# Kernel optimization log

Measured on AMD Instinct MI355X. Metric: run time of the kernel, lower is better.

The kernel has to match this reference:

```python
import jax, jax.numpy as jnp
import numpy as np

B, S, D = 4, 4096, 256

def setup_inputs() -> dict:
    key = jax.random.key(0)
    ks = jax.random.split(key, 7)
    s = 1.0 / np.sqrt(D)
    return {
        "x": jax.random.normal(ks[0], (B, S, D), dtype=jnp.float32),
        "Wq": jax.random.normal(ks[1], (D, D), dtype=jnp.float32) * s,
        "bq": jax.random.normal(ks[2], (D,), dtype=jnp.float32) * s,
        "Wk": jax.random.normal(ks[3], (D, D), dtype=jnp.float32) * s,
        "bk": jax.random.normal(ks[4], (D,), dtype=jnp.float32) * s,
        "Wv": jax.random.normal(ks[5], (D, D), dtype=jnp.float32) * s,
        "bv": jax.random.normal(ks[6], (D,), dtype=jnp.float32) * s,
    }

def reference(x, Wq, bq, Wk, bk, Wv, bv):
    # nn.Linear: y = x @ W.T + b
    q = jnp.einsum('bsd,ed->bse', x, Wq) + bq  # [B,S,D]
    k = jnp.einsum('bsd,ed->bse', x, Wk) + bk  # [B,S,D]
    v = jnp.einsum('bsd,ed->bse', x, Wv) + bv  # [B,S,D]
    scale = 1.0 / jnp.sqrt(jnp.float32(x.shape[-1]))
    scores = jnp.einsum('bqd,bkd->bqk', q, k) * scale  # [B,S,S]
    attn = jax.nn.softmax(scores, axis=-1)
    return jnp.einsum('bqk,bkd->bqd', attn, v)
```

## Files before the change

kernel.cpp:

```cpp
#include <hip/hip_runtime.h>

typedef __attribute__((ext_vector_type(8))) short bf16x8;
typedef __attribute__((ext_vector_type(4))) short bf16x4;
typedef __attribute__((ext_vector_type(4))) float f32x4;
typedef __attribute__((ext_vector_type(16))) float f32x16;

#define MFMA16(a,b,c) __builtin_amdgcn_mfma_f32_16x16x32_bf16((a),(b),(c),0,0,0)
#define MFMA32(a,b,c) __builtin_amdgcn_mfma_f32_32x32x16_bf16((a),(b),(c),0,0,0)

__device__ __forceinline__ short f2bf(float f) {
  union { float f; unsigned u; } v; v.f = f;
  unsigned r = v.u + 0x7FFFu + ((v.u >> 16) & 1u);
  return (short)(r >> 16);
}

__device__ __forceinline__ void async16(const void* g, void* l) {
  __builtin_amdgcn_global_load_lds(
      (const __attribute__((address_space(1))) unsigned*)g,
      (__attribute__((address_space(3))) unsigned*)l, 16, 0, 0);
}

__global__ void cvt_w_kernel(const float* __restrict__ Wq, const float* __restrict__ Wk,
                             const float* __restrict__ Wv, short* __restrict__ Wb) {
  int v = blockIdx.x * 256 + threadIdx.x;
  int z = v >> 13, r = v & 8191;
  const float* src = ((z == 0) ? Wq : (z == 1) ? Wk : Wv) + r * 8;
  float4 a = *(const float4*)src;
  float4 b = *(const float4*)(src + 4);
  bf16x8 h;
  h[0]=f2bf(a.x); h[1]=f2bf(a.y); h[2]=f2bf(a.z); h[3]=f2bf(a.w);
  h[4]=f2bf(b.x); h[5]=f2bf(b.y); h[6]=f2bf(b.z); h[7]=f2bf(b.w);
  *(bf16x8*)(Wb + z * 65536 + r * 8) = h;
}

__global__ __launch_bounds__(256, 1) void proj_kernel(
    const float* __restrict__ x, const short* __restrict__ Wb,
    const float* __restrict__ bq, const float* __restrict__ bk, const float* __restrict__ bv,
    short* __restrict__ Qb, short* __restrict__ Kb, short* __restrict__ VTb)
{
  __shared__ __attribute__((aligned(16))) char xs[32768];
  const int tid = threadIdx.x;
  const int lane = tid & 63;
  const int w = tid >> 6;
  const int l15 = lane & 15, lg = lane >> 4;
  const int m0 = blockIdx.x * 64;
  const int batch = m0 >> 12;
  const int s0 = m0 & 4095;

  #pragma unroll
  for (int c = 0; c < 8; ++c) {
    int v = c * 256 + tid;
    int row = v >> 5, u = v & 31;
    const float* g = x + (size_t)(m0 + row) * 256 + u * 8;
    float4 a = *(const float4*)g;
    float4 b = *(const float4*)(g + 4);
    bf16x8 h;
    h[0]=f2bf(a.x); h[1]=f2bf(a.y); h[2]=f2bf(a.z); h[3]=f2bf(a.w);
    h[4]=f2bf(b.x); h[5]=f2bf(b.y); h[6]=f2bf(b.z); h[7]=f2bf(b.w);
    *(bf16x8*)(xs + row * 512 + ((u ^ (row & 7)) * 16)) = h;
  }
  __syncthreads();

  for (int z = 0; z < 2; ++z) {
    const short* Wz = Wb + z * 65536;
    const float* bias = z ? bk : bq;
    short* Ob = z ? Kb : Qb;
    const float scl = z ? 1.0f : 0.0625f;
    bf16x8 wf[4][8];
    #pragma unroll
    for (int fc = 0; fc < 4; ++fc)
      #pragma unroll
      for (int ks = 0; ks < 8; ++ks)
        wf[fc][ks] = *(const bf16x8*)(Wz + (size_t)(w*64 + fc*16 + l15) * 256 + ks*32 + lg*8);
    float bb[4];
    #pragma unroll
    for (int fc = 0; fc < 4; ++fc) bb[fc] = bias[w*64 + fc*16 + l15];
    #pragma unroll
    for (int ms = 0; ms < 4; ++ms) {
      bf16x8 xa[8];
      #pragma unroll
      for (int ks = 0; ks < 8; ++ks) {
        int row = ms * 16 + l15;
        xa[ks] = *(const bf16x8*)(xs + row * 512 + (((ks*4 + lg) ^ (row & 7)) * 16));
      }
      f32x4 acc[4];
      #pragma unroll
      for (int fc = 0; fc < 4; ++fc) acc[fc] = (f32x4){0.f,0.f,0.f,0.f};
      #pragma unroll
      for (int ks = 0; ks < 8; ++ks)
        #pragma unroll
        for (int fc = 0; fc < 4; ++fc)
          acc[fc] = MFMA16(xa[ks], wf[fc][ks], acc[fc]);
      #pragma unroll
      for (int fc = 0; fc < 4; ++fc)
        #pragma unroll
        for (int r = 0; r < 4; ++r)
          Ob[(size_t)(m0 + ms*16 + lg*4 + r) * 256 + w*64 + fc*16 + l15] =
              f2bf((acc[fc][r] + bb[fc]) * scl);
    }
  }

  {
    const short* Wz = Wb + 2 * 65536;
    bf16x8 wf[4][8];
    #pragma unroll
    for (int fr = 0; fr < 4; ++fr)
      #pragma unroll
      for (int ks = 0; ks < 8; ++ks)
        wf[fr][ks] = *(const bf16x8*)(Wz + (size_t)(w*64 + fr*16 + l15) * 256 + ks*32 + lg*8);
    float bvr[4][4];
    #pragma unroll
    for (int fr = 0; fr < 4; ++fr)
      #pragma unroll
      for (int r = 0; r < 4; ++r) bvr[fr][r] = bv[w*64 + fr*16 + lg*4 + r];
    #pragma unroll
    for (int ms = 0; ms < 4; ++ms) {
      bf16x8 xa[8];
      #pragma unroll
      for (int ks = 0; ks < 8; ++ks) {
        int row = ms * 16 + l15;
        xa[ks] = *(const bf16x8*)(xs + row * 512 + (((ks*4 + lg) ^ (row & 7)) * 16));
      }
      f32x4 acc[4];
      #pragma unroll
      for (int fr = 0; fr < 4; ++fr) acc[fr] = (f32x4){0.f,0.f,0.f,0.f};
      #pragma unroll
      for (int ks = 0; ks < 8; ++ks)
        #pragma unroll
        for (int fr = 0; fr < 4; ++fr)
          acc[fr] = MFMA16(wf[fr][ks], xa[ks], acc[fr]);
      #pragma unroll
      for (int fr = 0; fr < 4; ++fr)
        #pragma unroll
        for (int r = 0; r < 4; ++r) {
          int e = w*64 + fr*16 + lg*4 + r;
          VTb[(size_t)(batch*256 + e) * 4096 + s0 + ms*16 + l15] = f2bf(acc[fr][r] + bvr[fr][r]);
        }
    }
  }
}

__global__ __launch_bounds__(512, 2) void attn_kernel(
    const short* __restrict__ Qb, const short* __restrict__ Kb,
    const short* __restrict__ VTb, float* __restrict__ Op, float* __restrict__ mlg)
{
  __shared__ __attribute__((aligned(16))) char smem[148480];
  const int tid = threadIdx.x;
  const int lane = tid & 63;
  const int w = tid >> 6;
  const int l31 = lane & 31, hi = lane >> 5;
  const int qs = w & 3, kh = w >> 2, dh = kh;

  const int b = blockIdx.x;
  const int xcd = b & 7;
  const int batch = xcd >> 1, ns = xcd & 1;
  const int qt = b >> 3;
  const int q0 = qt * 128;
  const int kvbase = ns * 2048;

  const char* Kg = (const char*)(Kb  + (size_t)batch * 4096 * 256);
  const char* Vg = (const char*)(VTb + (size_t)batch * 256 * 4096);

  bf16x8 qf[16];
  {
    const short* qrow = Qb + (size_t)(batch*4096 + q0 + qs*32 + l31) * 256;
    #pragma unroll
    for (int ks = 0; ks < 16; ++ks) qf[ks] = *(const bf16x8*)(qrow + ks*16 + hi*8);
  }

  f32x16 o[4];
  #pragma unroll
  for (int i = 0; i < 4; ++i)
    #pragma unroll
    for (int r = 0; r < 16; ++r) o[i][r] = 0.f;
  float m_run = -1e30f, l_run = 0.f;

  float* ml = (float*)(smem + 147456);
  char* pl = smem + 131072 + qs * 4096;

  auto stage = [&](int buf, int kv0) {
    char* kl = smem + buf * 32768;
    #pragma unroll
    for (int c = 0; c < 4; ++c) {
      int v = c * 512 + tid;
      int row = v >> 5, s = v & 31;
      async16(Kg + (size_t)(kv0 + row) * 512 + ((s ^ (row & 7)) * 16),
              kl + (c * 512 + w * 64) * 16);
    }
    char* vl = smem + 65536 + buf * 32768;
    #pragma unroll
    for (int c = 0; c < 4; ++c) {
      int v = c * 512 + tid;
      int row = v >> 3, s = v & 7;
      async16(Vg + (size_t)row * 8192 + (size_t)kv0 * 2 + ((s ^ (row & 7)) * 16),
              vl + (c * 512 + w * 64) * 16);
    }
  };

  stage(0, kvbase);
  __syncthreads();

  for (int t = 0; t < 32; ++t) {
    const int cur = t & 1;
    if (t < 31) stage(cur ^ 1, kvbase + (t + 1) * 64);

    const char* kl = smem + cur * 32768;
    const char* vl = smem + 65536 + cur * 32768;

    f32x16 st;
    #pragma unroll
    for (int r = 0; r < 16; ++r) st[r] = 0.f;
    #pragma unroll
    for (int ks = 0; ks < 16; ++ks) {
      int row = kh * 32 + l31;
      bf16x8 kf = *(const bf16x8*)(kl + row * 512 + (((ks*2 + hi) ^ (row & 7)) * 16));
      st = MFMA32(kf, qf[ks], st);
    }

    float mx = st[0];
    #pragma unroll
    for (int r = 1; r < 16; ++r) mx = fmaxf(mx, st[r]);
    mx = fmaxf(mx, __shfl_xor(mx, 32));
    if (!hi) ml[kh * 128 + qs * 32 + l31] = mx;
    asm volatile("s_waitcnt lgkmcnt(0)" ::: "memory");
    __builtin_amdgcn_s_barrier();
    float mo = ml[(kh ^ 1) * 128 + qs * 32 + l31];
    float m_new = fmaxf(m_run, fmaxf(mx, mo));
    if (m_new > m_run) {
      float alpha = __expf(m_run - m_new);
      l_run *= alpha;
      #pragma unroll
      for (int df = 0; df < 4; ++df) o[df] = o[df] * alpha;
      m_run = m_new;
    }
    float ps[16];
    float lsum = 0.f;
    #pragma unroll
    for (int r = 0; r < 16; ++r) { ps[r] = __expf(st[r] - m_run); lsum += ps[r]; }
    l_run += lsum;
    #pragma unroll
    for (int g = 0; g < 4; ++g) {
      bf16x4 pv;
      #pragma unroll
      for (int j = 0; j < 4; ++j) pv[j] = f2bf(ps[4*g + j]);
      int qd = kh * 8 + 2 * g + hi;
      int u8 = qd ^ ((l31 & 7) << 1);
      *(bf16x4*)(pl + l31 * 128 + u8 * 8) = pv;
    }
    asm volatile("s_waitcnt lgkmcnt(0)" ::: "memory");
    __builtin_amdgcn_s_barrier();

    #pragma unroll
    for (int ks = 0; ks < 4; ++ks) {
      int u8 = (ks * 4 + hi * 2) ^ ((l31 & 7) << 1);
      bf16x8 pa = *(const bf16x8*)(pl + l31 * 128 + u8 * 8);
      #pragma unroll
      for (int df = 0; df < 4; ++df) {
        int row = dh * 128 + df * 32 + l31;
        bf16x8 vb = *(const bf16x8*)(vl + row * 128 + (((ks*2 + hi) ^ (row & 7)) * 16));
        o[df] = MFMA32(vb, pa, o[df]);
      }
    }
    __syncthreads();
  }

  float lw = l_run + __shfl_xor(l_run, 32);
  if (!hi) ml[kh * 128 + qs * 32 + l31] = lw;
  asm volatile("s_waitcnt lgkmcnt(0)" ::: "memory");
  __builtin_amdgcn_s_barrier();
  float lt = ml[qs * 32 + l31] + ml[128 + qs * 32 + l31];
  const int qglob = batch * 4096 + q0 + qs * 32 + l31;
  float* op = Op + ((size_t)ns * 16384 + qglob) * 256;
  #pragma unroll
  for (int df = 0; df < 4; ++df)
    #pragma unroll
    for (int g = 0; g < 4; ++g) {
      float4 vv = {o[df][4*g], o[df][4*g+1], o[df][4*g+2], o[df][4*g+3]};
      *(float4*)(op + dh * 128 + df * 32 + 8 * g + 4 * hi) = vv;
    }
  if (kh == 0 && !hi) {
    mlg[((size_t)ns * 16384 + qglob) * 2]     = m_run;
    mlg[((size_t)ns * 16384 + qglob) * 2 + 1] = lt;
  }
}

__global__ void combine_kernel(const float* __restrict__ Op, const float* __restrict__ mlg,
                               float* __restrict__ out) {
  int idx = blockIdx.x * 256 + threadIdx.x;
  int row = idx >> 6, c = idx & 63;
  float m0 = mlg[row * 2],           l0 = mlg[row * 2 + 1];
  float m1 = mlg[(16384 + row) * 2], l1 = mlg[(16384 + row) * 2 + 1];
  float ms = fmaxf(m0, m1);
  float a0 = __expf(m0 - ms), a1 = __expf(m1 - ms);
  float inv = 1.0f / (l0 * a0 + l1 * a1);
  a0 *= inv; a1 *= inv;
  float4 p0 = *(const float4*)(Op + (size_t)row * 256 + c * 4);
  float4 p1 = *(const float4*)(Op + (size_t)(16384 + row) * 256 + c * 4);
  float4 r;
  r.x = p0.x * a0 + p1.x * a1;
  r.y = p0.y * a0 + p1.y * a1;
  r.z = p0.z * a0 + p1.z * a1;
  r.w = p0.w * a0 + p1.w * a1;
  *(float4*)(out + (size_t)row * 256 + c * 4) = r;
}

extern "C" void kernel_launch(void* const* d_in, const int* in_sizes, int n_in,
                              void* d_out, int out_size, void* d_ws, size_t ws_size,
                              hipStream_t stream) {
  const float* x  = (const float*)d_in[0];
  const float* Wq = (const float*)d_in[1];
  const float* bq = (const float*)d_in[2];
  const float* Wk = (const float*)d_in[3];
  const float* bk = (const float*)d_in[4];
  const float* Wv = (const float*)d_in[5];
  const float* bv = (const float*)d_in[6];
  float* out = (float*)d_out;

  char* ws = (char*)d_ws;
  short* Qb  = (short*)(ws);
  short* Kb  = (short*)(ws + 8388608);
  short* VTb = (short*)(ws + 16777216);
  short* Wb  = (short*)(ws + 25165824);
  float* Op  = (float*)(ws + 25559040);
  float* mlg = (float*)(ws + 59113472);

  cvt_w_kernel<<<dim3(96), dim3(256), 0, stream>>>(Wq, Wk, Wv, Wb);
  proj_kernel<<<dim3(256), dim3(256), 0, stream>>>(x, Wb, bq, bk, bv, Qb, Kb, VTb);
  attn_kernel<<<dim3(256), dim3(512), 0, stream>>>(Qb, Kb, VTb, Op, mlg);
  combine_kernel<<<dim3(4096), dim3(256), 0, stream>>>(Op, mlg, out);
}
```

Baseline: 191.0 us.

## Split KV across warp halves with register-resident P and bf16 partial outputs

```diff
diff --git a/kernel.cpp b/kernel.cpp
--- a/kernel.cpp
+++ b/kernel.cpp
@@ -13,7 +13,15 @@
   unsigned r = v.u + 0x7FFFu + ((v.u >> 16) & 1u);
   return (short)(r >> 16);
 }
-
+__device__ __forceinline__ float bf2f(short s) {
+  union { unsigned u; float f; } v; v.u = ((unsigned)(unsigned short)s) << 16;
+  return v.f;
+}
+__device__ __forceinline__ unsigned cvtpk(float lo, float hi) {
+  unsigned d;
+  asm("v_cvt_pk_bf16_f32 %0, %1, %2" : "=v"(d) : "v"(lo), "v"(hi));
+  return d;
+}
 __device__ __forceinline__ void async16(const void* g, void* l) {
   __builtin_amdgcn_global_load_lds(
       (const __attribute__((address_space(1))) unsigned*)g,
@@ -33,22 +41,22 @@
   *(bf16x8*)(Wb + z * 65536 + r * 8) = h;
 }
 
-__global__ __launch_bounds__(256, 1) void proj_kernel(
+__global__ __launch_bounds__(256, 2) void proj_kernel(
     const float* __restrict__ x, const short* __restrict__ Wb,
     const float* __restrict__ bq, const float* __restrict__ bk, const float* __restrict__ bv,
     short* __restrict__ Qb, short* __restrict__ Kb, short* __restrict__ VTb)
 {
-  __shared__ __attribute__((aligned(16))) char xs[32768];
+  __shared__ __attribute__((aligned(16))) char xs[65536];
   const int tid = threadIdx.x;
   const int lane = tid & 63;
   const int w = tid >> 6;
   const int l15 = lane & 15, lg = lane >> 4;
-  const int m0 = blockIdx.x * 64;
+  const int m0 = blockIdx.x * 128;
   const int batch = m0 >> 12;
   const int s0 = m0 & 4095;
 
   #pragma unroll
-  for (int c = 0; c < 8; ++c) {
+  for (int c = 0; c < 16; ++c) {
     int v = c * 256 + tid;
     int row = v >> 5, u = v & 31;
     const float* g = x + (size_t)(m0 + row) * 256 + u * 8;
@@ -61,95 +69,89 @@
   }
   __syncthreads();
 
-  for (int z = 0; z < 2; ++z) {
+  for (int z = 0; z < 3; ++z) {
     const short* Wz = Wb + z * 65536;
-    const float* bias = z ? bk : bq;
-    short* Ob = z ? Kb : Qb;
-    const float scl = z ? 1.0f : 0.0625f;
     bf16x8 wf[4][8];
     #pragma unroll
     for (int fc = 0; fc < 4; ++fc)
       #pragma unroll
       for (int ks = 0; ks < 8; ++ks)
         wf[fc][ks] = *(const bf16x8*)(Wz + (size_t)(w*64 + fc*16 + l15) * 256 + ks*32 + lg*8);
-    float bb[4];
-    #pragma unroll
-    for (int fc = 0; fc < 4; ++fc) bb[fc] = bias[w*64 + fc*16 + l15];
-    #pragma unroll
-    for (int ms = 0; ms < 4; ++ms) {
-      bf16x8 xa[8];
-      #pragma unroll
-      for (int ks = 0; ks < 8; ++ks) {
-        int row = ms * 16 + l15;
-        xa[ks] = *(const bf16x8*)(xs + row * 512 + (((ks*4 + lg) ^ (row & 7)) * 16));
-      }
-      f32x4 acc[4];
-      #pragma unroll
-      for (int fc = 0; fc < 4; ++fc) acc[fc] = (f32x4){0.f,0.f,0.f,0.f};
-      #pragma unroll
-      for (int ks = 0; ks < 8; ++ks)
+
+    if (z < 2) {
+      const float* bias = z ? bk : bq;
+      short* Ob = z ? Kb : Qb;
+      const float scl = z ? 1.0f : 0.0625f;
+      float bb[4];
+      #pragma unroll
+      for (int fc = 0; fc < 4; ++fc) bb[fc] = bias[w*64 + fc*16 + l15];
+      #pragma unroll
+      for (int ms = 0; ms < 8; ++ms) {
+        bf16x8 xa[8];
+        #pragma unroll
+        for (int ks = 0; ks < 8; ++ks) {
+          int row = ms * 16 + l15;
+          xa[ks] = *(const bf16x8*)(xs + row * 512 + (((ks*4 + lg) ^ (row & 7)) * 16));
+        }
+        f32x4 acc[4];
+        #pragma unroll
+        for (int fc = 0; fc < 4; ++fc) acc[fc] = (f32x4){0.f,0.f,0.f,0.f};
+        #pragma unroll
+        for (int ks = 0; ks < 8; ++ks)
+          #pragma unroll
+          for (int fc = 0; fc < 4; ++fc)
+            acc[fc] = MFMA16(xa[ks], wf[fc][ks], acc[fc]);
         #pragma unroll
         for (int fc = 0; fc < 4; ++fc)
-          acc[fc] = MFMA16(xa[ks], wf[fc][ks], acc[fc]);
-      #pragma unroll
-      for (int fc = 0; fc < 4; ++fc)
-        #pragma unroll
-        for (int r = 0; r < 4; ++r)
-          Ob[(size_t)(m0 + ms*16 + lg*4 + r) * 256 + w*64 + fc*16 + l15] =
-              f2bf((acc[fc][r] + bb[fc]) * scl);
-    }
-  }
-
-  {
-    const short* Wz = Wb + 2 * 65536;
-    bf16x8 wf[4][8];
-    #pragma unroll
-    for (int fr = 0; fr < 4; ++fr)
-      #pragma unroll
-      for (int ks = 0; ks < 8; ++ks)
-        wf[fr][ks] = *(const bf16x8*)(Wz + (size_t)(w*64 + fr*16 + l15) * 256 + ks*32 + lg*8);
-    float bvr[4][4];
-    #pragma unroll
-    for (int fr = 0; fr < 4; ++fr)
-      #pragma unroll
-      for (int r = 0; r < 4; ++r) bvr[fr][r] = bv[w*64 + fr*16 + lg*4 + r];
-    #pragma unroll
-    for (int ms = 0; ms < 4; ++ms) {
-      bf16x8 xa[8];
-      #pragma unroll
-      for (int ks = 0; ks < 8; ++ks) {
-        int row = ms * 16 + l15;
-        xa[ks] = *(const bf16x8*)(xs + row * 512 + (((ks*4 + lg) ^ (row & 7)) * 16));
-      }
-      f32x4 acc[4];
-      #pragma unroll
-      for (int fr = 0; fr < 4; ++fr) acc[fr] = (f32x4){0.f,0.f,0.f,0.f};
-      #pragma unroll
-      for (int ks = 0; ks < 8; ++ks)
+          #pragma unroll
+          for (int r = 0; r < 4; ++r)
+            Ob[(size_t)(m0 + ms*16 + lg*4 + r) * 256 + w*64 + fc*16 + l15] =
+                f2bf((acc[fc][r] + bb[fc]) * scl);
+      }
+    } else {
+      float bvr[4][4];
+      #pragma unroll
+      for (int fr = 0; fr < 4; ++fr)
+        #pragma unroll
+        for (int r = 0; r < 4; ++r) bvr[fr][r] = bv[w*64 + fr*16 + lg*4 + r];
+      #pragma unroll
+      for (int ms = 0; ms < 8; ++ms) {
+        bf16x8 xa[8];
+        #pragma unroll
+        for (int ks = 0; ks < 8; ++ks) {
+          int row = ms * 16 + l15;
+          xa[ks] = *(const bf16x8*)(xs + row * 512 + (((ks*4 + lg) ^ (row & 7)) * 16));
+        }
+        f32x4 acc[4];
+        #pragma unroll
+        for (int fr = 0; fr < 4; ++fr) acc[fr] = (f32x4){0.f,0.f,0.f,0.f};
+        #pragma unroll
+        for (int ks = 0; ks < 8; ++ks)
+          #pragma unroll
+          for (int fr = 0; fr < 4; ++fr)
+            acc[fr] = MFMA16(wf[fr][ks], xa[ks], acc[fr]);
         #pragma unroll
         for (int fr = 0; fr < 4; ++fr)
-          acc[fr] = MFMA16(wf[fr][ks], xa[ks], acc[fr]);
-      #pragma unroll
-      for (int fr = 0; fr < 4; ++fr)
-        #pragma unroll
-        for (int r = 0; r < 4; ++r) {
-          int e = w*64 + fr*16 + lg*4 + r;
-          VTb[(size_t)(batch*256 + e) * 4096 + s0 + ms*16 + l15] = f2bf(acc[fr][r] + bvr[fr][r]);
-        }
+          #pragma unroll
+          for (int r = 0; r < 4; ++r) {
+            int e = w*64 + fr*16 + lg*4 + r;
+            VTb[(size_t)(batch*256 + e) * 4096 + s0 + ms*16 + l15] = f2bf(acc[fr][r] + bvr[fr][r]);
+          }
+      }
     }
   }
 }
 
 __global__ __launch_bounds__(512, 2) void attn_kernel(
     const short* __restrict__ Qb, const short* __restrict__ Kb,
-    const short* __restrict__ VTb, float* __restrict__ Op, float* __restrict__ mlg)
+    const short* __restrict__ VTb, short* __restrict__ Op, float* __restrict__ mlg)
 {
-  __shared__ __attribute__((aligned(16))) char smem[148480];
+  __shared__ __attribute__((aligned(16))) char smem[131072];
   const int tid = threadIdx.x;
   const int lane = tid & 63;
   const int w = tid >> 6;
   const int l31 = lane & 31, hi = lane >> 5;
-  const int qs = w & 3, kh = w >> 2, dh = kh;
+  const int qs = w & 3, kh = w >> 2;
 
   const int b = blockIdx.x;
   const int xcd = b & 7;
@@ -168,15 +170,12 @@
     for (int ks = 0; ks < 16; ++ks) qf[ks] = *(const bf16x8*)(qrow + ks*16 + hi*8);
   }
 
-  f32x16 o[4];
+  f32x16 o[8];
   #pragma unroll
-  for (int i = 0; i < 4; ++i)
+  for (int i = 0; i < 8; ++i)
     #pragma unroll
     for (int r = 0; r < 16; ++r) o[i][r] = 0.f;
   float m_run = -1e30f, l_run = 0.f;
-
-  float* ml = (float*)(smem + 147456);
-  char* pl = smem + 131072 + qs * 4096;
 
   auto stage = [&](int buf, int kv0) {
     char* kl = smem + buf * 32768;
@@ -210,98 +209,141 @@
     f32x16 st;
     #pragma unroll
     for (int r = 0; r < 16; ++r) st[r] = 0.f;
+    __builtin_amdgcn_s_setprio(1);
     #pragma unroll
     for (int ks = 0; ks < 16; ++ks) {
       int row = kh * 32 + l31;
       bf16x8 kf = *(const bf16x8*)(kl + row * 512 + (((ks*2 + hi) ^ (row & 7)) * 16));
       st = MFMA32(kf, qf[ks], st);
     }
+    __builtin_amdgcn_s_setprio(0);
 
     float mx = st[0];
     #pragma unroll
     for (int r = 1; r < 16; ++r) mx = fmaxf(mx, st[r]);
     mx = fmaxf(mx, __shfl_xor(mx, 32));
-    if (!hi) ml[kh * 128 + qs * 32 + l31] = mx;
-    asm volatile("s_waitcnt lgkmcnt(0)" ::: "memory");
-    __builtin_amdgcn_s_barrier();
-    float mo = ml[(kh ^ 1) * 128 + qs * 32 + l31];
-    float m_new = fmaxf(m_run, fmaxf(mx, mo));
+    float m_new = fmaxf(m_run, mx);
     if (m_new > m_run) {
       float alpha = __expf(m_run - m_new);
       l_run *= alpha;
       #pragma unroll
-      for (int df = 0; df < 4; ++df) o[df] = o[df] * alpha;
+      for (int df = 0; df < 8; ++df) o[df] = o[df] * alpha;
       m_run = m_new;
     }
-    float ps[16];
     float lsum = 0.f;
     #pragma unroll
-    for (int r = 0; r < 16; ++r) { ps[r] = __expf(st[r] - m_run); lsum += ps[r]; }
+    for (int r = 0; r < 16; ++r) { st[r] = __expf(st[r] - m_run); lsum += st[r]; }
     l_run += lsum;
-    #pragma unroll
-    for (int g = 0; g < 4; ++g) {
-      bf16x4 pv;
-      #pragma unroll
-      for (int j = 0; j < 4; ++j) pv[j] = f2bf(ps[4*g + j]);
-      int qd = kh * 8 + 2 * g + hi;
-      int u8 = qd ^ ((l31 & 7) << 1);
-      *(bf16x4*)(pl + l31 * 128 + u8 * 8) = pv;
-    }
-    asm volatile("s_waitcnt lgkmcnt(0)" ::: "memory");
-    __builtin_amdgcn_s_barrier();
-
-    #pragma unroll
-    for (int ks = 0; ks < 4; ++ks) {
-      int u8 = (ks * 4 + hi * 2) ^ ((l31 & 7) << 1);
-      bf16x8 pa = *(const bf16x8*)(pl + l31 * 128 + u8 * 8);
-      #pragma unroll
-      for (int df = 0; df < 4; ++df) {
-        int row = dh * 128 + df * 32 + l31;
-        bf16x8 vb = *(const bf16x8*)(vl + row * 128 + (((ks*2 + hi) ^ (row & 7)) * 16));
-        o[df] = MFMA32(vb, pa, o[df]);
-      }
-    }
+
+    bf16x8 pa[2];
+    #pragma unroll
+    for (int kvf = 0; kvf < 2; ++kvf) {
+      float s0_ = st[8*kvf+0], s1_ = st[8*kvf+1], s2_ = st[8*kvf+2], s3_ = st[8*kvf+3];
+      float s4_ = st[8*kvf+4], s5_ = st[8*kvf+5], s6_ = st[8*kvf+6], s7_ = st[8*kvf+7];
+      unsigned X  = cvtpk(s0_, s1_);
+      unsigned X2 = cvtpk(s2_, s3_);
+      unsigned Y  = cvtpk(s4_, s5_);
+      unsigned Y2 = cvtpk(s6_, s7_);
+      unsigned Xs  = __shfl_xor((int)X, 32);
+      unsigned X2s = __shfl_xor((int)X2, 32);
+      unsigned Ys  = __shfl_xor((int)Y, 32);
+      unsigned Y2s = __shfl_xor((int)Y2, 32);
+      union { unsigned u[4]; bf16x8 v; } fr;
+      fr.u[0] = hi ? Ys  : X;
+      fr.u[1] = hi ? Y2s : X2;
+      fr.u[2] = hi ? Y   : Xs;
+      fr.u[3] = hi ? Y2  : X2s;
+      pa[kvf] = fr.v;
+    }
+
+    __builtin_amdgcn_s_setprio(1);
+    #pragma unroll
+    for (int kvf = 0; kvf < 2; ++kvf) {
+      #pragma unroll
+      for (int df = 0; df < 8; ++df) {
+        int row = df * 32 + l31;
+        int u = (kh*2 + kvf) * 2 + hi;
+        bf16x8 vb = *(const bf16x8*)(vl + row * 128 + ((u ^ (row & 7)) * 16));
+        o[df] = MFMA32(vb, pa[kvf], o[df]);
+      }
+    }
+    __builtin_amdgcn_s_setprio(0);
+
     __syncthreads();
   }
 
-  float lw = l_run + __shfl_xor(l_run, 32);
-  if (!hi) ml[kh * 128 + qs * 32 + l31] = lw;
-  asm volatile("s_waitcnt lgkmcnt(0)" ::: "memory");
-  __builtin_amdgcn_s_barrier();
-  float lt = ml[qs * 32 + l31] + ml[128 + qs * 32 + l31];
-  const int qglob = batch * 4096 + q0 + qs * 32 + l31;
-  float* op = Op + ((size_t)ns * 16384 + qglob) * 256;
-  #pragma unroll
-  for (int df = 0; df < 4; ++df)
-    #pragma unroll
-    for (int g = 0; g < 4; ++g) {
-      float4 vv = {o[df][4*g], o[df][4*g+1], o[df][4*g+2], o[df][4*g+3]};
-      *(float4*)(op + dh * 128 + df * 32 + 8 * g + 4 * hi) = vv;
-    }
-  if (kh == 0 && !hi) {
-    mlg[((size_t)ns * 16384 + qglob) * 2]     = m_run;
-    mlg[((size_t)ns * 16384 + qglob) * 2 + 1] = lt;
-  }
-}
-
-__global__ void combine_kernel(const float* __restrict__ Op, const float* __restrict__ mlg,
+  float lt = l_run + __shfl_xor(l_run, 32);
+  float* ml = (float*)smem;
+  if (!hi) {
+    float2 v = {m_run, lt};
+    *(float2*)(ml + ((kh*4 + qs)*32 + l31)*2) = v;
+  }
+  __syncthreads();
+  float2 other = *(const float2*)(ml + (((kh^1)*4 + qs)*32 + l31)*2);
+  float m_star = fmaxf(m_run, other.x);
+  float a_own = __expf(m_run - m_star);
+  float l_star = a_own * lt + __expf(other.x - m_star) * other.y;
+  char* xt = smem + 4096 + qs * 16384;
+
+  if (kh == 1) {
+    #pragma unroll
+    for (int df = 0; df < 8; ++df)
+      #pragma unroll
+      for (int g = 0; g < 4; ++g) {
+        bf16x4 pv;
+        #pragma unroll
+        for (int c = 0; c < 4; ++c) pv[c] = f2bf(o[df][4*g + c] * a_own);
+        int u = (df*32 + 8*g + 4*hi) >> 2;
+        *(bf16x4*)(xt + l31*512 + ((u ^ (l31 & 7)) * 8)) = pv;
+      }
+  }
+  __syncthreads();
+  if (kh == 0) {
+    const int qglob = batch*4096 + q0 + qs*32 + l31;
+    short* op = Op + ((size_t)ns * 16384 + qglob) * 256;
+    #pragma unroll
+    for (int df = 0; df < 8; ++df)
+      #pragma unroll
+      for (int g = 0; g < 4; ++g) {
+        int u = (df*32 + 8*g + 4*hi) >> 2;
+        bf16x4 p1 = *(const bf16x4*)(xt + l31*512 + ((u ^ (l31 & 7)) * 8));
+        bf16x4 pv;
+        #pragma unroll
+        for (int c = 0; c < 4; ++c)
+          pv[c] = f2bf(o[df][4*g + c] * a_own + bf2f(p1[c]));
+        *(bf16x4*)(op + df*32 + 8*g + 4*hi) = pv;
+      }
+    if (!hi) {
+      mlg[((size_t)ns*16384 + qglob)*2]     = m_star;
+      mlg[((size_t)ns*16384 + qglob)*2 + 1] = l_star;
+    }
+  }
+}
+
+__global__ void combine_kernel(const short* __restrict__ Op, const float* __restrict__ mlg,
                                float* __restrict__ out) {
   int idx = blockIdx.x * 256 + threadIdx.x;
-  int row = idx >> 6, c = idx & 63;
+  int row = idx >> 5, c = idx & 31;
   float m0 = mlg[row * 2],           l0 = mlg[row * 2 + 1];
   float m1 = mlg[(16384 + row) * 2], l1 = mlg[(16384 + row) * 2 + 1];
   float ms = fmaxf(m0, m1);
   float a0 = __expf(m0 - ms), a1 = __expf(m1 - ms);
   float inv = 1.0f / (l0 * a0 + l1 * a1);
   a0 *= inv; a1 *= inv;
-  float4 p0 = *(const float4*)(Op + (size_t)row * 256 + c * 4);
-  float4 p1 = *(const float4*)(Op + (size_t)(16384 + row) * 256 + c * 4);
-  float4 r;
-  r.x = p0.x * a0 + p1.x * a1;
-  r.y = p0.y * a0 + p1.y * a1;
-  r.z = p0.z * a0 + p1.z * a1;
-  r.w = p0.w * a0 + p1.w * a1;
-  *(float4*)(out + (size_t)row * 256 + c * 4) = r;
+  bf16x8 v0 = *(const bf16x8*)(Op + (size_t)row * 256 + c * 8);
+  bf16x8 v1 = *(const bf16x8*)(Op + (size_t)(16384 + row) * 256 + c * 8);
+  float4 r0, r1;
+  r0.x = a0*bf2f(v0[0]) + a1*bf2f(v1[0]);
+  r0.y = a0*bf2f(v0[1]) + a1*bf2f(v1[1]);
+  r0.z = a0*bf2f(v0[2]) + a1*bf2f(v1[2]);
+  r0.w = a0*bf2f(v0[3]) + a1*bf2f(v1[3]);
+  r1.x = a0*bf2f(v0[4]) + a1*bf2f(v1[4]);
+  r1.y = a0*bf2f(v0[5]) + a1*bf2f(v1[5]);
+  r1.z = a0*bf2f(v0[6]) + a1*bf2f(v1[6]);
+  r1.w = a0*bf2f(v0[7]) + a1*bf2f(v1[7]);
+  float* po = out + (size_t)row * 256 + c * 8;
+  *(float4*)po = r0;
+  *(float4*)(po + 4) = r1;
 }
 
 extern "C" void kernel_launch(void* const* d_in, const int* in_sizes, int n_in,
@@ -321,11 +363,11 @@
   short* Kb  = (short*)(ws + 8388608);
   short* VTb = (short*)(ws + 16777216);
   short* Wb  = (short*)(ws + 25165824);
-  float* Op  = (float*)(ws + 25559040);
-  float* mlg = (float*)(ws + 59113472);
+  float* mlg = (float*)(ws + 25559040);
+  short* Op  = (short*)(ws + 25821184);
 
   cvt_w_kernel<<<dim3(96), dim3(256), 0, stream>>>(Wq, Wk, Wv, Wb);
-  proj_kernel<<<dim3(256), dim3(256), 0, stream>>>(x, Wb, bq, bk, bv, Qb, Kb, VTb);
+  proj_kernel<<<dim3(128), dim3(256), 0, stream>>>(x, Wb, bq, bk, bv, Qb, Kb, VTb);
   attn_kernel<<<dim3(256), dim3(512), 0, stream>>>(Qb, Kb, VTb, Op, mlg);
-  combine_kernel<<<dim3(4096), dim3(256), 0, stream>>>(Op, mlg, out);
-}
+  combine_kernel<<<dim3(2048), dim3(256), 0, stream>>>(Op, mlg, out);
+}
```

After: 214.4 us. 12.2% more time.
